# Optimization experiments

Measured on AMD Instinct MI355X. Metric: run time of the kernel, lower is better.

## Reference

```python
import jax, jax.numpy as jnp
import numpy as np

B, S, IN_DIM = 2, 2048, 1024
DIMS, QH, KVH = 1024, 16, 4
HD = DIMS // QH          # head_dims = 64
G = QH // KVH            # groups = 4


def setup_inputs() -> dict:
    key = jax.random.key(0)
    k1, k2, k3, k4, k5, k6 = jax.random.split(key, 6)
    scale = 0.02
    q_in = jax.random.normal(k1, (B, S, IN_DIM), dtype=jnp.float32)
    kv_in = jax.random.normal(k2, (B, S, IN_DIM), dtype=jnp.float32)
    # causal mask (True = attend)
    mask = jnp.tril(jnp.ones((S, S), dtype=bool))
    Wq = jax.random.normal(k3, (IN_DIM, QH, HD), dtype=jnp.float32) * scale
    Wk = jax.random.normal(k4, (IN_DIM, KVH, HD), dtype=jnp.float32) * scale
    Wv = jax.random.normal(k5, (IN_DIM, KVH, HD), dtype=jnp.float32) * scale
    Wo = jax.random.normal(k6, (KVH * HD, IN_DIM), dtype=jnp.float32) * scale
    return {"q_in": q_in, "kv_in": kv_in, "mask": mask,
            "Wq": Wq, "Wk": Wk, "Wv": Wv, "Wo": Wo}


def reference(q_in, kv_in, mask, Wq, Wk, Wv, Wo):
    b, s, _ = q_in.shape
    # projections (DenseGeneral, no bias)
    q = jnp.einsum('bsi,ihd->bshd', q_in, Wq)   # [B,S,QH,HD]
    k = jnp.einsum('bsi,ihd->bshd', kv_in, Wk)  # [B,S,KVH,HD]
    v = jnp.einsum('bsi,ihd->bshd', kv_in, Wv)  # [B,S,KVH,HD]
    # rearrange '... s (h g) d -> ... g h s d' with g=G (h outer, g inner),
    # then einsum '... g h s d, ... h a d -> ... h s a' sums over g.
    # Equivalent (and cheaper): sum q over the group axis first.
    q_g = q.reshape(b, s, KVH, G, HD).sum(axis=3)        # [B,S,KVH,HD]
    q_g = jnp.transpose(q_g, (0, 2, 1, 3))               # [B,KVH,S,HD]
    k = jnp.transpose(k, (0, 2, 1, 3))                   # [B,KVH,S,HD]
    v = jnp.transpose(v, (0, 2, 1, 3))                   # [B,KVH,S,HD]
    scores = jnp.einsum('bhsd,bhad->bhsa', q_g, k)       # [B,KVH,S,S]
    scores = jnp.where(mask[None, None, :, :], scores, -jnp.inf)
    attn = jax.nn.softmax(scores / (HD ** 0.5), axis=-1)
    out = jnp.einsum('bhsa,bhad->bhsd', attn, v)         # [B,KVH,S,HD]
    out = jnp.transpose(out, (0, 2, 1, 3)).reshape(b, s, KVH * HD)
    return out @ Wo                                      # [B,S,IN_DIM]
```

## Files before the change

### kernel.cpp

```cpp
#include <hip/hip_runtime.h>
#include <hip/hip_bf16.h>

#define SS 2048

typedef __attribute__((ext_vector_type(8))) short bf16x8;
typedef __attribute__((ext_vector_type(4))) float f32x4;

__device__ __forceinline__ short f2bf(float f){
    unsigned u = __float_as_uint(f);
    u += 0x7fff + ((u >> 16) & 1);
    return (short)(u >> 16);
}

__global__ __launch_bounds__(256) void k_prep_w(const float* __restrict__ Wq,
                                                const float* __restrict__ Wk,
                                                const float* __restrict__ Wv,
                                                const float* __restrict__ Wo,
                                                short* __restrict__ WcatT,
                                                short* __restrict__ WoT){
    __shared__ float Ts[64][65];
    const int bx = blockIdx.x;
    const int r  = threadIdx.x >> 2;
    const int cq = (threadIdx.x & 3) * 16;
    if (bx < 192) {
        const int ktile = bx & 15, ntile = bx >> 4;
        const int k0 = ktile * 64, n0 = ntile * 64;
        if (ntile < 4) {
            const float* base = Wq + (size_t)(k0 + r) * 1024 + ntile * 256;
            #pragma unroll
            for (int i = 0; i < 16; i += 4) {
                float4 a = *(const float4*)(base + cq + i);
                float4 b = *(const float4*)(base + 64 + cq + i);
                float4 c = *(const float4*)(base + 128 + cq + i);
                float4 d = *(const float4*)(base + 192 + cq + i);
                Ts[r][cq+i]   = 0.125f * (a.x + b.x + c.x + d.x);
                Ts[r][cq+i+1] = 0.125f * (a.y + b.y + c.y + d.y);
                Ts[r][cq+i+2] = 0.125f * (a.z + b.z + c.z + d.z);
                Ts[r][cq+i+3] = 0.125f * (a.w + b.w + c.w + d.w);
            }
        } else {
            const float* W = (ntile < 8) ? Wk : Wv;
            const float* base = W + (size_t)(k0 + r) * 256 + (ntile & 3) * 64;
            #pragma unroll
            for (int i = 0; i < 16; i += 4) {
                float4 a = *(const float4*)(base + cq + i);
                Ts[r][cq+i] = a.x; Ts[r][cq+i+1] = a.y;
                Ts[r][cq+i+2] = a.z; Ts[r][cq+i+3] = a.w;
            }
        }
        __syncthreads();
        short tmp[16];
        #pragma unroll
        for (int i = 0; i < 16; ++i) tmp[i] = f2bf(Ts[cq+i][r]);
        short* dst = WcatT + (size_t)(n0 + r) * 1024 + k0 + cq;
        *(bf16x8*)dst       = *(bf16x8*)&tmp[0];
        *(bf16x8*)(dst + 8) = *(bf16x8*)&tmp[8];
    } else {
        const int b2 = bx - 192;
        const int ktile = b2 & 3, ntile = b2 >> 2;
        const int k0 = ktile * 64, n0 = ntile * 64;
        const float* base = Wo + (size_t)(k0 + r) * 1024 + n0;
        #pragma unroll
        for (int i = 0; i < 16; i += 4) {
            float4 a = *(const float4*)(base + cq + i);
            Ts[r][cq+i] = a.x; Ts[r][cq+i+1] = a.y;
            Ts[r][cq+i+2] = a.z; Ts[r][cq+i+3] = a.w;
        }
        __syncthreads();
        short tmp[16];
        #pragma unroll
        for (int i = 0; i < 16; ++i) tmp[i] = f2bf(Ts[cq+i][r]);
        short* dst = WoT + (size_t)(n0 + r) * 256 + k0 + cq;
        *(bf16x8*)dst       = *(bf16x8*)&tmp[0];
        *(bf16x8*)(dst + 8) = *(bf16x8*)&tmp[8];
    }
}

__global__ __launch_bounds__(256) void k_prep_x(const float* __restrict__ q_in,
                                                const float* __restrict__ kv_in,
                                                short* __restrict__ xq,
                                                short* __restrict__ xkv){
    const float* src = blockIdx.y ? kv_in : q_in;
    short* dst = blockIdx.y ? xkv : xq;
    int i = (blockIdx.x * 256 + threadIdx.x) * 4;
    float4 f = *(const float4*)(src + i);
    short4 o;
    o.x = f2bf(f.x); o.y = f2bf(f.y); o.z = f2bf(f.z); o.w = f2bf(f.w);
    *(short4*)(dst + i) = o;
}

__global__ __launch_bounds__(256) void k_gemm1(const short* __restrict__ xq,
                                               const short* __restrict__ xkv,
                                               const short* __restrict__ WcatT,
                                               short* __restrict__ pqk,
                                               short* __restrict__ vt){
    const int m0 = blockIdx.x * 128;
    const int n0 = blockIdx.y * 128;
    const short* X = (n0 < 256) ? xq : xkv;
    const int tid = threadIdx.x;
    const int wave = tid >> 6, lane = tid & 63, quad = lane >> 4, l16 = lane & 15;
    const int wrow = (wave & 1) * 64, wcol = (wave >> 1) * 64;
    const int r = tid >> 2, cc = (tid & 3) * 16;

    __shared__ short As[128][72];
    __shared__ short Bs[128][72];

    f32x4 acc[4][4];
    #pragma unroll
    for (int tm = 0; tm < 4; ++tm)
        #pragma unroll
        for (int tn = 0; tn < 4; ++tn) acc[tm][tn] = f32x4{0.f,0.f,0.f,0.f};

    for (int k0 = 0; k0 < 1024; k0 += 64) {
        const short* a0 = X + (size_t)(m0 + r) * 1024 + k0 + cc;
        const short* a1 = X + (size_t)(m0 + r + 64) * 1024 + k0 + cc;
        const short* b0 = WcatT + (size_t)(n0 + r) * 1024 + k0 + cc;
        const short* b1 = WcatT + (size_t)(n0 + r + 64) * 1024 + k0 + cc;
        *(bf16x8*)&As[r][cc]          = *(const bf16x8*)a0;
        *(bf16x8*)&As[r][cc + 8]      = *(const bf16x8*)(a0 + 8);
        *(bf16x8*)&As[r + 64][cc]     = *(const bf16x8*)a1;
        *(bf16x8*)&As[r + 64][cc + 8] = *(const bf16x8*)(a1 + 8);
        *(bf16x8*)&Bs[r][cc]          = *(const bf16x8*)b0;
        *(bf16x8*)&Bs[r][cc + 8]      = *(const bf16x8*)(b0 + 8);
        *(bf16x8*)&Bs[r + 64][cc]     = *(const bf16x8*)b1;
        *(bf16x8*)&Bs[r + 64][cc + 8] = *(const bf16x8*)(b1 + 8);
        __syncthreads();
        #pragma unroll
        for (int ks = 0; ks < 2; ++ks) {
            bf16x8 a[4];
            #pragma unroll
            for (int tm = 0; tm < 4; ++tm)
                a[tm] = *(bf16x8*)&As[wrow + tm * 16 + l16][ks * 32 + quad * 8];
            #pragma unroll
            for (int tn = 0; tn < 4; ++tn) {
                bf16x8 b = *(bf16x8*)&Bs[wcol + tn * 16 + l16][ks * 32 + quad * 8];
                #pragma unroll
                for (int tm = 0; tm < 4; ++tm)
                    acc[tm][tn] = __builtin_amdgcn_mfma_f32_16x16x32_bf16(a[tm], b, acc[tm][tn], 0, 0, 0);
            }
        }
        __syncthreads();
    }
    if (n0 < 512) {
        #pragma unroll
        for (int tm = 0; tm < 4; ++tm) {
            const int mrow = m0 + wrow + tm * 16 + quad * 4;
            #pragma unroll
            for (int tn = 0; tn < 4; ++tn) {
                const int col = n0 + wcol + tn * 16 + l16;
                #pragma unroll
                for (int rg = 0; rg < 4; ++rg)
                    pqk[(size_t)(mrow + rg) * 512 + col] = f2bf(acc[tm][tn][rg]);
            }
        }
    } else {
        #pragma unroll
        for (int tm = 0; tm < 4; ++tm) {
            const int mrow = m0 + wrow + tm * 16 + quad * 4;
            #pragma unroll
            for (int tn = 0; tn < 4; ++tn) {
                const int colv = n0 - 512 + wcol + tn * 16 + l16;
                const int vh = colv >> 6, d = colv & 63;
                #pragma unroll
                for (int rg = 0; rg < 4; ++rg) {
                    int m = mrow + rg, batch = m >> 11, s = m & 2047;
                    vt[((size_t)((batch * 4 + vh) * 64 + d)) * 2048 + s] = f2bf(acc[tm][tn][rg]);
                }
            }
        }
    }
}

__global__ __launch_bounds__(256) void k_attn4(const short* __restrict__ pqk,
                                               const short* __restrict__ vt,
                                               float* __restrict__ Op,
                                               float* __restrict__ Lp,
                                               int nsplit){
    const int bx = blockIdx.x;
    const int qt = 31 - (bx / nsplit);
    const int s  = bx - (bx / nsplit) * nsplit;
    const int kv = blockIdx.y, batch = blockIdx.z;
    const int tid = threadIdx.x;
    const int wave = tid >> 6, lane = tid & 63, quad = lane >> 4, l16 = lane & 15;
    const int r = tid >> 2, c = (tid & 3) * 16;
    const int part = (((batch * 4 + kv) * 32 + qt) * nsplit + s);

    __shared__ short Ks[64][72];
    __shared__ short Vs[64][72];
    __shared__ short Ps[64][72];

    const size_t qrow = (size_t)(batch * SS + qt * 64 + wave * 16 + l16);
    bf16x8 aq0 = *(const bf16x8*)(pqk + qrow * 512 + kv * 64 + quad * 8);
    bf16x8 aq1 = *(const bf16x8*)(pqk + qrow * 512 + kv * 64 + 32 + quad * 8);

    f32x4 accO[4];
    #pragma unroll
    for (int t = 0; t < 4; ++t) accO[t] = f32x4{0.f, 0.f, 0.f, 0.f};
    float lrow[4] = {0.f, 0.f, 0.f, 0.f};

    bf16x8 rk0, rk1, rv0, rv1;
    int kt = s;
    if (kt <= qt) {
        const short* ksrc = pqk + (size_t)(batch * SS + kt * 64 + r) * 512 + 256 + kv * 64 + c;
        rk0 = *(const bf16x8*)ksrc; rk1 = *(const bf16x8*)(ksrc + 8);
        const short* vsrc = vt + ((size_t)((batch * 4 + kv) * 64 + r)) * 2048 + kt * 64 + c;
        rv0 = *(const bf16x8*)vsrc; rv1 = *(const bf16x8*)(vsrc + 8);
    }
    for (; kt <= qt; kt += nsplit) {
        *(bf16x8*)&Ks[r][c]     = rk0;
        *(bf16x8*)&Ks[r][c + 8] = rk1;
        *(bf16x8*)&Vs[r][c]     = rv0;
        *(bf16x8*)&Vs[r][c + 8] = rv1;
        __syncthreads();
        if (kt + nsplit <= qt) {
            const short* ksrc = pqk + (size_t)(batch * SS + (kt + nsplit) * 64 + r) * 512 + 256 + kv * 64 + c;
            rk0 = *(const bf16x8*)ksrc; rk1 = *(const bf16x8*)(ksrc + 8);
            const short* vsrc = vt + ((size_t)((batch * 4 + kv) * 64 + r)) * 2048 + (kt + nsplit) * 64 + c;
            rv0 = *(const bf16x8*)vsrc; rv1 = *(const bf16x8*)(vsrc + 8);
        }

        f32x4 sc[4];
        #pragma unroll
        for (int t = 0; t < 4; ++t) sc[t] = f32x4{0.f, 0.f, 0.f, 0.f};
        #pragma unroll
        for (int ks = 0; ks < 2; ++ks) {
            bf16x8 a = ks ? aq1 : aq0;
            #pragma unroll
            for (int t = 0; t < 4; ++t) {
                bf16x8 b = *(bf16x8*)&Ks[t * 16 + l16][ks * 32 + quad * 8];
                sc[t] = __builtin_amdgcn_mfma_f32_16x16x32_bf16(a, b, sc[t], 0, 0, 0);
            }
        }
        if (kt == qt) {
            #pragma unroll
            for (int t = 0; t < 4; ++t) {
                int colg = t * 16 + l16;
                #pragma unroll
                for (int rg = 0; rg < 4; ++rg)
                    if (colg > wave * 16 + quad * 4 + rg) sc[t][rg] = -1e30f;
            }
        }
        #pragma unroll
        for (int t = 0; t < 4; ++t) {
            #pragma unroll
            for (int rg = 0; rg < 4; ++rg) {
                float p = __expf(sc[t][rg]);
                lrow[rg] += p;
                Ps[wave * 16 + quad * 4 + rg][t * 16 + l16] = f2bf(p);
            }
        }
        #pragma unroll
        for (int ks = 0; ks < 2; ++ks) {
            bf16x8 ap = *(bf16x8*)&Ps[wave * 16 + l16][ks * 32 + quad * 8];
            #pragma unroll
            for (int t = 0; t < 4; ++t) {
                bf16x8 bv = *(bf16x8*)&Vs[t * 16 + l16][ks * 32 + quad * 8];
                accO[t] = __builtin_amdgcn_mfma_f32_16x16x32_bf16(ap, bv, accO[t], 0, 0, 0);
            }
        }
        __syncthreads();
    }
    #pragma unroll
    for (int rg = 0; rg < 4; ++rg) {
        float l = lrow[rg];
        l += __shfl_xor(l, 1);
        l += __shfl_xor(l, 2);
        l += __shfl_xor(l, 4);
        l += __shfl_xor(l, 8);
        lrow[rg] = l;
    }
    #pragma unroll
    for (int rg = 0; rg < 4; ++rg) {
        int row = wave * 16 + quad * 4 + rg;
        #pragma unroll
        for (int t = 0; t < 4; ++t)
            Op[(size_t)part * 4096 + row * 64 + t * 16 + l16] = accO[t][rg];
    }
    if (l16 == 0) {
        #pragma unroll
        for (int rg = 0; rg < 4; ++rg)
            Lp[part * 64 + (wave * 16 + quad * 4 + rg)] = lrow[rg];
    }
}

__global__ __launch_bounds__(256) void k_combine(const float* __restrict__ Op,
                                                 const float* __restrict__ Lp,
                                                 short* __restrict__ ao,
                                                 int nsplit){
    const int qt = blockIdx.x, kv = blockIdx.y, batch = blockIdx.z;
    const int tid = threadIdx.x;
    const int rr = tid >> 2, cs = (tid & 3) * 16;
    const int pbase = ((batch * 4 + kv) * 32 + qt) * nsplit;
    float lsum = 0.f;
    for (int i = 0; i < nsplit; ++i) lsum += Lp[(pbase + i) * 64 + rr];
    float inv = 1.f / lsum;
    float o[16];
    #pragma unroll
    for (int j = 0; j < 16; ++j) o[j] = 0.f;
    for (int i = 0; i < nsplit; ++i) {
        const float* src = Op + (size_t)(pbase + i) * 4096 + rr * 64 + cs;
        #pragma unroll
        for (int j = 0; j < 16; j += 4) {
            float4 f = *(const float4*)(src + j);
            o[j] += f.x; o[j+1] += f.y; o[j+2] += f.z; o[j+3] += f.w;
        }
    }
    short* dst = ao + (size_t)(batch * SS + qt * 64 + rr) * 256 + kv * 64 + cs;
    #pragma unroll
    for (int j = 0; j < 16; ++j)
        dst[j] = f2bf(o[j] * inv);
}

__global__ __launch_bounds__(256) void k_gemm2(const short* __restrict__ ao,
                                               const short* __restrict__ WoT,
                                               float* __restrict__ out){
    const int m0 = blockIdx.x * 128;
    const int n0 = blockIdx.y * 128;
    const int tid = threadIdx.x;
    const int wave = tid >> 6, lane = tid & 63, quad = lane >> 4, l16 = lane & 15;
    const int wrow = (wave & 1) * 64, wcol = (wave >> 1) * 64;
    const int r = tid >> 2, cc = (tid & 3) * 16;

    __shared__ short As[128][72];
    __shared__ short Bs[128][72];

    f32x4 acc[4][4];
    #pragma unroll
    for (int tm = 0; tm < 4; ++tm)
        #pragma unroll
        for (int tn = 0; tn < 4; ++tn) acc[tm][tn] = f32x4{0.f,0.f,0.f,0.f};

    for (int k0 = 0; k0 < 256; k0 += 64) {
        const short* a0 = ao + (size_t)(m0 + r) * 256 + k0 + cc;
        const short* a1 = ao + (size_t)(m0 + r + 64) * 256 + k0 + cc;
        const short* b0 = WoT + (size_t)(n0 + r) * 256 + k0 + cc;
        const short* b1 = WoT + (size_t)(n0 + r + 64) * 256 + k0 + cc;
        *(bf16x8*)&As[r][cc]          = *(const bf16x8*)a0;
        *(bf16x8*)&As[r][cc + 8]      = *(const bf16x8*)(a0 + 8);
        *(bf16x8*)&As[r + 64][cc]     = *(const bf16x8*)a1;
        *(bf16x8*)&As[r + 64][cc + 8] = *(const bf16x8*)(a1 + 8);
        *(bf16x8*)&Bs[r][cc]          = *(const bf16x8*)b0;
        *(bf16x8*)&Bs[r][cc + 8]      = *(const bf16x8*)(b0 + 8);
        *(bf16x8*)&Bs[r + 64][cc]     = *(const bf16x8*)b1;
        *(bf16x8*)&Bs[r + 64][cc + 8] = *(const bf16x8*)(b1 + 8);
        __syncthreads();
        #pragma unroll
        for (int ks = 0; ks < 2; ++ks) {
            bf16x8 a[4];
            #pragma unroll
            for (int tm = 0; tm < 4; ++tm)
                a[tm] = *(bf16x8*)&As[wrow + tm * 16 + l16][ks * 32 + quad * 8];
            #pragma unroll
            for (int tn = 0; tn < 4; ++tn) {
                bf16x8 b = *(bf16x8*)&Bs[wcol + tn * 16 + l16][ks * 32 + quad * 8];
                #pragma unroll
                for (int tm = 0; tm < 4; ++tm)
                    acc[tm][tn] = __builtin_amdgcn_mfma_f32_16x16x32_bf16(a[tm], b, acc[tm][tn], 0, 0, 0);
            }
        }
        __syncthreads();
    }
    #pragma unroll
    for (int tm = 0; tm < 4; ++tm) {
        const int mrow = m0 + wrow + tm * 16 + quad * 4;
        #pragma unroll
        for (int tn = 0; tn < 4; ++tn) {
            const int col = n0 + wcol + tn * 16 + l16;
            #pragma unroll
            for (int rg = 0; rg < 4; ++rg)
                out[(size_t)(mrow + rg) * 1024 + col] = acc[tm][tn][rg];
        }
    }
}

extern "C" void kernel_launch(void* const* d_in, const int* in_sizes, int n_in,
                              void* d_out, int out_size, void* d_ws, size_t ws_size,
                              hipStream_t stream) {
    const float* q_in  = (const float*)d_in[0];
    const float* kv_in = (const float*)d_in[1];
    int wqi = 3;
    for (int i = 2; i < n_in; ++i)
        if (in_sizes[i] == 1024 * 16 * 64) { wqi = i; break; }
    const float* Wq = (const float*)d_in[wqi];
    const float* Wk = (const float*)d_in[wqi + 1];
    const float* Wv = (const float*)d_in[wqi + 2];
    const float* Wo = (const float*)d_in[wqi + 3];
    float* out = (float*)d_out;

    char* ws = (char*)d_ws;
    short* WcatT = (short*)(ws);
    short* WoT   = (short*)(ws + 1572864);
    short* ao    = (short*)(ws + 2097152);
    short* pqk   = (short*)(ws + 4194304);
    short* vt    = (short*)(ws + 8388608);
    float* Lp    = (float*)(ws + 10485760);
    short* xq    = (short*)(ws + 12582912);
    short* xkv   = (short*)(ws + 20971520);
    float* Op    = (float*)(ws + 33554432);
    const int nsplit = 4;

    hipLaunchKernelGGL(k_prep_w,  dim3(256),     dim3(256), 0, stream,
                       Wq, Wk, Wv, Wo, WcatT, WoT);
    hipLaunchKernelGGL(k_prep_x,  dim3(4096, 2), dim3(256), 0, stream,
                       q_in, kv_in, xq, xkv);
    hipLaunchKernelGGL(k_gemm1,   dim3(32, 6),   dim3(256), 0, stream,
                       xq, xkv, WcatT, pqk, vt);
    hipLaunchKernelGGL(k_attn4,   dim3(32 * nsplit, 4, 2), dim3(256), 0, stream,
                       pqk, vt, Op, Lp, nsplit);
    hipLaunchKernelGGL(k_combine, dim3(32, 4, 2), dim3(256), 0, stream,
                       Op, Lp, ao, nsplit);
    hipLaunchKernelGGL(k_gemm2,   dim3(32, 8),   dim3(256), 0, stream,
                       ao, WoT, out);
}
```

Before: 165.6 us.

## Fuse fp32-to-bf16 input conversion into projection GEMM and prefetch tiles in registers

Drops the separate input conversion kernel and has the first GEMM load fp32 activations and convert them to bf16 while staging. Both GEMMs now prefetch the next K tile into registers during the current tile's MFMA work. The attention split count is doubled for more parallelism. This removes a full write and read of bf16 activation copies, at the cost of reading fp32 input per N-block, more register pressure, and larger partial buffers for the combine step.

```diff
diff --git a/kernel.cpp b/kernel.cpp
--- a/kernel.cpp
+++ b/kernel.cpp
@@ -76,27 +76,14 @@
     }
 }
 
-__global__ __launch_bounds__(256) void k_prep_x(const float* __restrict__ q_in,
-                                                const float* __restrict__ kv_in,
-                                                short* __restrict__ xq,
-                                                short* __restrict__ xkv){
-    const float* src = blockIdx.y ? kv_in : q_in;
-    short* dst = blockIdx.y ? xkv : xq;
-    int i = (blockIdx.x * 256 + threadIdx.x) * 4;
-    float4 f = *(const float4*)(src + i);
-    short4 o;
-    o.x = f2bf(f.x); o.y = f2bf(f.y); o.z = f2bf(f.z); o.w = f2bf(f.w);
-    *(short4*)(dst + i) = o;
-}
-
-__global__ __launch_bounds__(256) void k_gemm1(const short* __restrict__ xq,
-                                               const short* __restrict__ xkv,
+__global__ __launch_bounds__(256) void k_gemm1(const float* __restrict__ q_in,
+                                               const float* __restrict__ kv_in,
                                                const short* __restrict__ WcatT,
                                                short* __restrict__ pqk,
                                                short* __restrict__ vt){
     const int m0 = blockIdx.x * 128;
     const int n0 = blockIdx.y * 128;
-    const short* X = (n0 < 256) ? xq : xkv;
+    const float* X = (n0 < 256) ? q_in : kv_in;
     const int tid = threadIdx.x;
     const int wave = tid >> 6, lane = tid & 63, quad = lane >> 4, l16 = lane & 15;
     const int wrow = (wave & 1) * 64, wcol = (wave >> 1) * 64;
@@ -111,20 +98,49 @@
         #pragma unroll
         for (int tn = 0; tn < 4; ++tn) acc[tm][tn] = f32x4{0.f,0.f,0.f,0.f};
 
+    short ta0[16], ta1[16];
+    bf16x8 rb0, rb1, rb2, rb3;
+    {
+        const float* a0 = X + (size_t)(m0 + r) * 1024 + cc;
+        const float* a1 = a0 + (size_t)64 * 1024;
+        #pragma unroll
+        for (int i = 0; i < 16; i += 4) {
+            float4 f = *(const float4*)(a0 + i);
+            ta0[i] = f2bf(f.x); ta0[i+1] = f2bf(f.y); ta0[i+2] = f2bf(f.z); ta0[i+3] = f2bf(f.w);
+            float4 g = *(const float4*)(a1 + i);
+            ta1[i] = f2bf(g.x); ta1[i+1] = f2bf(g.y); ta1[i+2] = f2bf(g.z); ta1[i+3] = f2bf(g.w);
+        }
+        const short* b0 = WcatT + (size_t)(n0 + r) * 1024 + cc;
+        const short* b1 = b0 + (size_t)64 * 1024;
+        rb0 = *(const bf16x8*)b0; rb1 = *(const bf16x8*)(b0 + 8);
+        rb2 = *(const bf16x8*)b1; rb3 = *(const bf16x8*)(b1 + 8);
+    }
+
     for (int k0 = 0; k0 < 1024; k0 += 64) {
-        const short* a0 = X + (size_t)(m0 + r) * 1024 + k0 + cc;
-        const short* a1 = X + (size_t)(m0 + r + 64) * 1024 + k0 + cc;
-        const short* b0 = WcatT + (size_t)(n0 + r) * 1024 + k0 + cc;
-        const short* b1 = WcatT + (size_t)(n0 + r + 64) * 1024 + k0 + cc;
-        *(bf16x8*)&As[r][cc]          = *(const bf16x8*)a0;
-        *(bf16x8*)&As[r][cc + 8]      = *(const bf16x8*)(a0 + 8);
-        *(bf16x8*)&As[r + 64][cc]     = *(const bf16x8*)a1;
-        *(bf16x8*)&As[r + 64][cc + 8] = *(const bf16x8*)(a1 + 8);
-        *(bf16x8*)&Bs[r][cc]          = *(const bf16x8*)b0;
-        *(bf16x8*)&Bs[r][cc + 8]      = *(const bf16x8*)(b0 + 8);
-        *(bf16x8*)&Bs[r + 64][cc]     = *(const bf16x8*)b1;
-        *(bf16x8*)&Bs[r + 64][cc + 8] = *(const bf16x8*)(b1 + 8);
-        __syncthreads();
+        *(bf16x8*)&As[r][cc]          = *(bf16x8*)&ta0[0];
+        *(bf16x8*)&As[r][cc + 8]      = *(bf16x8*)&ta0[8];
+        *(bf16x8*)&As[r + 64][cc]     = *(bf16x8*)&ta1[0];
+        *(bf16x8*)&As[r + 64][cc + 8] = *(bf16x8*)&ta1[8];
+        *(bf16x8*)&Bs[r][cc]          = rb0;
+        *(bf16x8*)&Bs[r][cc + 8]      = rb1;
+        *(bf16x8*)&Bs[r + 64][cc]     = rb2;
+        *(bf16x8*)&Bs[r + 64][cc + 8] = rb3;
+        __syncthreads();
+        if (k0 + 64 < 1024) {
+            const float* a0 = X + (size_t)(m0 + r) * 1024 + k0 + 64 + cc;
+            const float* a1 = a0 + (size_t)64 * 1024;
+            #pragma unroll
+            for (int i = 0; i < 16; i += 4) {
+                float4 f = *(const float4*)(a0 + i);
+                ta0[i] = f2bf(f.x); ta0[i+1] = f2bf(f.y); ta0[i+2] = f2bf(f.z); ta0[i+3] = f2bf(f.w);
+                float4 g = *(const float4*)(a1 + i);
+                ta1[i] = f2bf(g.x); ta1[i+1] = f2bf(g.y); ta1[i+2] = f2bf(g.z); ta1[i+3] = f2bf(g.w);
+            }
+            const short* b0 = WcatT + (size_t)(n0 + r) * 1024 + k0 + 64 + cc;
+            const short* b1 = b0 + (size_t)64 * 1024;
+            rb0 = *(const bf16x8*)b0; rb1 = *(const bf16x8*)(b0 + 8);
+            rb2 = *(const bf16x8*)b1; rb3 = *(const bf16x8*)(b1 + 8);
+        }
         #pragma unroll
         for (int ks = 0; ks < 2; ++ks) {
             bf16x8 a[4];
@@ -330,20 +346,37 @@
         #pragma unroll
         for (int tn = 0; tn < 4; ++tn) acc[tm][tn] = f32x4{0.f,0.f,0.f,0.f};
 
+    bf16x8 ra0, ra1, ra2, ra3, rb0, rb1, rb2, rb3;
+    {
+        const short* a0 = ao + (size_t)(m0 + r) * 256 + cc;
+        const short* a1 = a0 + (size_t)64 * 256;
+        const short* b0 = WoT + (size_t)(n0 + r) * 256 + cc;
+        const short* b1 = b0 + (size_t)64 * 256;
+        ra0 = *(const bf16x8*)a0; ra1 = *(const bf16x8*)(a0 + 8);
+        ra2 = *(const bf16x8*)a1; ra3 = *(const bf16x8*)(a1 + 8);
+        rb0 = *(const bf16x8*)b0; rb1 = *(const bf16x8*)(b0 + 8);
+        rb2 = *(const bf16x8*)b1; rb3 = *(const bf16x8*)(b1 + 8);
+    }
     for (int k0 = 0; k0 < 256; k0 += 64) {
-        const short* a0 = ao + (size_t)(m0 + r) * 256 + k0 + cc;
-        const short* a1 = ao + (size_t)(m0 + r + 64) * 256 + k0 + cc;
-        const short* b0 = WoT + (size_t)(n0 + r) * 256 + k0 + cc;
-        const short* b1 = WoT + (size_t)(n0 + r + 64) * 256 + k0 + cc;
-        *(bf16x8*)&As[r][cc]          = *(const bf16x8*)a0;
-        *(bf16x8*)&As[r][cc + 8]      = *(const bf16x8*)(a0 + 8);
-        *(bf16x8*)&As[r + 64][cc]     = *(const bf16x8*)a1;
-        *(bf16x8*)&As[r + 64][cc + 8] = *(const bf16x8*)(a1 + 8);
-        *(bf16x8*)&Bs[r][cc]          = *(const bf16x8*)b0;
-        *(bf16x8*)&Bs[r][cc + 8]      = *(const bf16x8*)(b0 + 8);
-        *(bf16x8*)&Bs[r + 64][cc]     = *(const bf16x8*)b1;
-        *(bf16x8*)&Bs[r + 64][cc + 8] = *(const bf16x8*)(b1 + 8);
-        __syncthreads();
+        *(bf16x8*)&As[r][cc]          = ra0;
+        *(bf16x8*)&As[r][cc + 8]      = ra1;
+        *(bf16x8*)&As[r + 64][cc]     = ra2;
+        *(bf16x8*)&As[r + 64][cc + 8] = ra3;
+        *(bf16x8*)&Bs[r][cc]          = rb0;
+        *(bf16x8*)&Bs[r][cc + 8]      = rb1;
+        *(bf16x8*)&Bs[r + 64][cc]     = rb2;
+        *(bf16x8*)&Bs[r + 64][cc + 8] = rb3;
+        __syncthreads();
+        if (k0 + 64 < 256) {
+            const short* a0 = ao + (size_t)(m0 + r) * 256 + k0 + 64 + cc;
+            const short* a1 = a0 + (size_t)64 * 256;
+            const short* b0 = WoT + (size_t)(n0 + r) * 256 + k0 + 64 + cc;
+            const short* b1 = b0 + (size_t)64 * 256;
+            ra0 = *(const bf16x8*)a0; ra1 = *(const bf16x8*)(a0 + 8);
+            ra2 = *(const bf16x8*)a1; ra3 = *(const bf16x8*)(a1 + 8);
+            rb0 = *(const bf16x8*)b0; rb1 = *(const bf16x8*)(b0 + 8);
+            rb2 = *(const bf16x8*)b1; rb3 = *(const bf16x8*)(b1 + 8);
+        }
         #pragma unroll
         for (int ks = 0; ks < 2; ++ks) {
             bf16x8 a[4];
@@ -394,17 +427,13 @@
     short* pqk   = (short*)(ws + 4194304);
     short* vt    = (short*)(ws + 8388608);
     float* Lp    = (float*)(ws + 10485760);
-    short* xq    = (short*)(ws + 12582912);
-    short* xkv   = (short*)(ws + 20971520);
     float* Op    = (float*)(ws + 33554432);
-    const int nsplit = 4;
+    const int nsplit = 8;
 
     hipLaunchKernelGGL(k_prep_w,  dim3(256),     dim3(256), 0, stream,
                        Wq, Wk, Wv, Wo, WcatT, WoT);
-    hipLaunchKernelGGL(k_prep_x,  dim3(4096, 2), dim3(256), 0, stream,
-                       q_in, kv_in, xq, xkv);
     hipLaunchKernelGGL(k_gemm1,   dim3(32, 6),   dim3(256), 0, stream,
-                       xq, xkv, WcatT, pqk, vt);
+                       q_in, kv_in, WcatT, pqk, vt);
     hipLaunchKernelGGL(k_attn4,   dim3(32 * nsplit, 4, 2), dim3(256), 0, stream,
                        pqk, vt, Op, Lp, nsplit);
     hipLaunchKernelGGL(k_combine, dim3(32, 4, 2), dim3(256), 0, stream,
```

After: 161.2 us. 2.7% less time.
